# Optimization experiments

Hardware: AMD Instinct MI355X
Metric: run time of the kernel (lower is better)

Reference implementation:

```python
import jax, jax.numpy as jnp
import numpy as np

B, S, H, E, TOP_K = 4, 4096, 4096, 64, 2

def setup_inputs() -> dict:
    key = jax.random.key(0)
    k1, k2 = jax.random.split(key)
    hidden_states = jax.random.normal(k1, (B, S, H), dtype=jnp.float32)
    gate_weight = jax.random.normal(k2, (E, H), dtype=jnp.float32) * (H ** -0.5)
    return {"hidden_states": hidden_states, "gate_weight": gate_weight}

def reference(hidden_states, gate_weight):
    # gate: logits[b,s,e] = hidden[b,s,h] @ W[e,h]^T (nn.Linear, no bias)
    router_logits = jnp.einsum('bsh,eh->bse', hidden_states, gate_weight)
    router_probs = jax.nn.softmax(router_logits, axis=-1)
    # top-k over experts, then renormalize the selected weights
    expert_weights, expert_indices = jax.lax.top_k(router_probs, TOP_K)
    expert_weights = expert_weights / jnp.sum(expert_weights, axis=-1, keepdims=True)
    return (router_probs, expert_indices, expert_weights)
```

## Files before the change

kernel.cpp:

```cpp
#include <hip/hip_runtime.h>
#include <math.h>

#define TOKENS 16384
#define HDIM 4096
#define NE 64

#define BM 64
#define BK 32
#define KSPLIT 8
#define KSLICE (HDIM / KSPLIT)
#define LDSP 68

__global__ __launch_bounds__(256, 4) void router_gemm(const float* __restrict__ A,
                                                      const float* __restrict__ W,
                                                      float* __restrict__ P) {
  __shared__ float As[BK * LDSP];
  __shared__ float Ws[BK * LDSP];

  const int tid = threadIdx.x;
  const int bt = blockIdx.x;
  const int ks = blockIdx.y;

  const int sr = tid >> 2;
  const int sc = (tid & 3) * 4;

  const float* Ab = A + (size_t)(bt * BM + sr) * HDIM + (size_t)ks * KSLICE + sc;
  const float* Wb = W + (size_t)sr * HDIM + (size_t)ks * KSLICE + sc;

  const int tx = tid & 15;
  const int ty = tid >> 4;

  float acc[4][4];
#pragma unroll
  for (int i = 0; i < 4; ++i)
#pragma unroll
    for (int j = 0; j < 4; ++j) acc[i][j] = 0.f;

  float4 a0 = *(const float4*)(Ab);
  float4 a1 = *(const float4*)(Ab + 16);
  float4 w0 = *(const float4*)(Wb);
  float4 w1 = *(const float4*)(Wb + 16);

  for (int kc = 0; kc < KSLICE; kc += BK) {
    As[(sc + 0) * LDSP + sr] = a0.x;
    As[(sc + 1) * LDSP + sr] = a0.y;
    As[(sc + 2) * LDSP + sr] = a0.z;
    As[(sc + 3) * LDSP + sr] = a0.w;
    As[(sc + 16) * LDSP + sr] = a1.x;
    As[(sc + 17) * LDSP + sr] = a1.y;
    As[(sc + 18) * LDSP + sr] = a1.z;
    As[(sc + 19) * LDSP + sr] = a1.w;
    Ws[(sc + 0) * LDSP + sr] = w0.x;
    Ws[(sc + 1) * LDSP + sr] = w0.y;
    Ws[(sc + 2) * LDSP + sr] = w0.z;
    Ws[(sc + 3) * LDSP + sr] = w0.w;
    Ws[(sc + 16) * LDSP + sr] = w1.x;
    Ws[(sc + 17) * LDSP + sr] = w1.y;
    Ws[(sc + 18) * LDSP + sr] = w1.z;
    Ws[(sc + 19) * LDSP + sr] = w1.w;
    __syncthreads();

    if (kc + BK < KSLICE) {
      a0 = *(const float4*)(Ab + kc + BK);
      a1 = *(const float4*)(Ab + kc + BK + 16);
      w0 = *(const float4*)(Wb + kc + BK);
      w1 = *(const float4*)(Wb + kc + BK + 16);
    }

#pragma unroll
    for (int k = 0; k < BK; ++k) {
      float4 av = *(const float4*)&As[k * LDSP + ty * 4];
      float4 wv = *(const float4*)&Ws[k * LDSP + tx * 4];
      const float a[4] = {av.x, av.y, av.z, av.w};
      const float w[4] = {wv.x, wv.y, wv.z, wv.w};
#pragma unroll
      for (int i = 0; i < 4; ++i)
#pragma unroll
        for (int j = 0; j < 4; ++j) acc[i][j] = fmaf(a[i], w[j], acc[i][j]);
    }
    __syncthreads();
  }

  float* Pb = P + ((size_t)ks * TOKENS + (size_t)bt * BM + ty * 4) * NE + tx * 4;
#pragma unroll
  for (int i = 0; i < 4; ++i)
    *(float4*)(Pb + (size_t)i * NE) =
        make_float4(acc[i][0], acc[i][1], acc[i][2], acc[i][3]);
}

__global__ __launch_bounds__(256) void router_finalize(const float* __restrict__ P,
                                                       float* __restrict__ out) {
  const int lane = threadIdx.x & 63;
  const int wave = threadIdx.x >> 6;
  const int tok = blockIdx.x * 4 + wave;

  float l = 0.f;
#pragma unroll
  for (int s = 0; s < KSPLIT; ++s)
    l += P[((size_t)s * TOKENS + tok) * NE + lane];

  float m = l;
#pragma unroll
  for (int off = 32; off >= 1; off >>= 1) m = fmaxf(m, __shfl_xor(m, off, 64));

  const float e = expf(l - m);
  float sum = e;
#pragma unroll
  for (int off = 32; off >= 1; off >>= 1) sum += __shfl_xor(sum, off, 64);

  const float p = e / sum;
  out[(size_t)tok * NE + lane] = p;

  float m0 = p;
#pragma unroll
  for (int off = 32; off >= 1; off >>= 1) m0 = fmaxf(m0, __shfl_xor(m0, off, 64));
  const unsigned long long b0 = __ballot(p == m0);
  const int i0 = __ffsll(b0) - 1;

  const float pm = (lane == i0) ? -1.f : p;
  float m1 = pm;
#pragma unroll
  for (int off = 32; off >= 1; off >>= 1) m1 = fmaxf(m1, __shfl_xor(m1, off, 64));
  const unsigned long long b1 = __ballot(pm == m1);
  const int i1 = __ffsll(b1) - 1;

  if (lane == 0) {
    float* idxo = out + (size_t)TOKENS * NE + (size_t)tok * 2;
    idxo[0] = (float)i0;
    idxo[1] = (float)i1;
    float* wo = out + (size_t)TOKENS * NE + (size_t)TOKENS * 2 + (size_t)tok * 2;
    const float d = m0 + m1;
    wo[0] = m0 / d;
    wo[1] = m1 / d;
  }
}

extern "C" void kernel_launch(void* const* d_in, const int* in_sizes, int n_in,
                              void* d_out, int out_size, void* d_ws, size_t ws_size,
                              hipStream_t stream) {
  const float* A = (const float*)d_in[0];
  const float* W = (const float*)d_in[1];
  float* out = (float*)d_out;
  float* P = (float*)d_ws;

  dim3 gridA(TOKENS / BM, KSPLIT);
  router_gemm<<<gridA, 256, 0, stream>>>(A, W, P);
  router_finalize<<<TOKENS / 4, 256, 0, stream>>>(P, out);
}
```

Measured before the change: 397.4 us.

## Fuse router GEMM and softmax/top-k into one kernel with in-block K split

Replaces the 8-way split-K GEMM plus separate finalize kernel with a single kernel. Each 512-thread block covers 64 tokens and splits K across two 256-thread halves, then reduces the two partial sums in shared memory. Softmax and top-2 selection run in the same block straight from LDS. This removes the workspace round trip and the second launch. In exchange the grid shrinks to 256 blocks with a longer serial K loop, which lowers parallelism and latency hiding.

```diff
diff --git a/kernel.cpp b/kernel.cpp
--- a/kernel.cpp
+++ b/kernel.cpp
@@ -7,28 +7,32 @@
 
 #define BM 64
 #define BK 32
-#define KSPLIT 8
-#define KSLICE (HDIM / KSPLIT)
+#define NKG 2
+#define KSLICE (HDIM / NKG)
 #define LDSP 68
+#define TILE (BK * LDSP)
 
-__global__ __launch_bounds__(256, 4) void router_gemm(const float* __restrict__ A,
-                                                      const float* __restrict__ W,
-                                                      float* __restrict__ P) {
-  __shared__ float As[BK * LDSP];
-  __shared__ float Ws[BK * LDSP];
+__global__ __launch_bounds__(512, 2) void router_fused(const float* __restrict__ A,
+                                                       const float* __restrict__ W,
+                                                       float* __restrict__ out) {
+  __shared__ float smem[NKG * 2 * TILE];
 
   const int tid = threadIdx.x;
+  const int kg = tid >> 8;
+  const int t = tid & 255;
   const int bt = blockIdx.x;
-  const int ks = blockIdx.y;
 
-  const int sr = tid >> 2;
-  const int sc = (tid & 3) * 4;
+  const int sr = t >> 2;
+  const int sc = (t & 3) * 4;
 
-  const float* Ab = A + (size_t)(bt * BM + sr) * HDIM + (size_t)ks * KSLICE + sc;
-  const float* Wb = W + (size_t)sr * HDIM + (size_t)ks * KSLICE + sc;
+  const float* Ab = A + (size_t)(bt * BM + sr) * HDIM + (size_t)kg * KSLICE + sc;
+  const float* Wb = W + (size_t)sr * HDIM + (size_t)kg * KSLICE + sc;
 
-  const int tx = tid & 15;
-  const int ty = tid >> 4;
+  float* As = smem + kg * (2 * TILE);
+  float* Ws = As + TILE;
+
+  const int tx = t & 15;
+  const int ty = t >> 4;
 
   float acc[4][4];
 #pragma unroll
@@ -81,57 +85,67 @@
     __syncthreads();
   }
 
-  float* Pb = P + ((size_t)ks * TOKENS + (size_t)bt * BM + ty * 4) * NE + tx * 4;
+  float* L = smem;
+  if (kg == 0) {
 #pragma unroll
-  for (int i = 0; i < 4; ++i)
-    *(float4*)(Pb + (size_t)i * NE) =
-        make_float4(acc[i][0], acc[i][1], acc[i][2], acc[i][3]);
-}
+    for (int i = 0; i < 4; ++i)
+      *(float4*)&L[(ty * 4 + i) * LDSP + tx * 4] =
+          make_float4(acc[i][0], acc[i][1], acc[i][2], acc[i][3]);
+  }
+  __syncthreads();
+  if (kg == 1) {
+#pragma unroll
+    for (int i = 0; i < 4; ++i) {
+      float4* p = (float4*)&L[(ty * 4 + i) * LDSP + tx * 4];
+      float4 v = *p;
+      *p = make_float4(v.x + acc[i][0], v.y + acc[i][1], v.z + acc[i][2],
+                       v.w + acc[i][3]);
+    }
+  }
+  __syncthreads();
 
-__global__ __launch_bounds__(256) void router_finalize(const float* __restrict__ P,
-                                                       float* __restrict__ out) {
-  const int lane = threadIdx.x & 63;
-  const int wave = threadIdx.x >> 6;
-  const int tok = blockIdx.x * 4 + wave;
+  const int lane = tid & 63;
+  const int wv8 = tid >> 6;
+#pragma unroll
+  for (int r = 0; r < 8; ++r) {
+    const int lt = wv8 * 8 + r;
+    const int tok = bt * BM + lt;
+    const float l = L[lt * LDSP + lane];
 
-  float l = 0.f;
+    float m = l;
 #pragma unroll
-  for (int s = 0; s < KSPLIT; ++s)
-    l += P[((size_t)s * TOKENS + tok) * NE + lane];
+    for (int off = 32; off >= 1; off >>= 1) m = fmaxf(m, __shfl_xor(m, off, 64));
 
-  float m = l;
+    const float e = expf(l - m);
+    float sum = e;
 #pragma unroll
-  for (int off = 32; off >= 1; off >>= 1) m = fmaxf(m, __shfl_xor(m, off, 64));
+    for (int off = 32; off >= 1; off >>= 1) sum += __shfl_xor(sum, off, 64);
 
-  const float e = expf(l - m);
-  float sum = e;
+    const float p = e / sum;
+    out[(size_t)tok * NE + lane] = p;
+
+    float m0 = p;
 #pragma unroll
-  for (int off = 32; off >= 1; off >>= 1) sum += __shfl_xor(sum, off, 64);
+    for (int off = 32; off >= 1; off >>= 1) m0 = fmaxf(m0, __shfl_xor(m0, off, 64));
+    const unsigned long long b0 = __ballot(p == m0);
+    const int i0 = __ffsll(b0) - 1;
 
-  const float p = e / sum;
-  out[(size_t)tok * NE + lane] = p;
+    const float pm = (lane == i0) ? -1.f : p;
+    float m1 = pm;
+#pragma unroll
+    for (int off = 32; off >= 1; off >>= 1) m1 = fmaxf(m1, __shfl_xor(m1, off, 64));
+    const unsigned long long b1 = __ballot(pm == m1);
+    const int i1 = __ffsll(b1) - 1;
 
-  float m0 = p;
-#pragma unroll
-  for (int off = 32; off >= 1; off >>= 1) m0 = fmaxf(m0, __shfl_xor(m0, off, 64));
-  const unsigned long long b0 = __ballot(p == m0);
-  const int i0 = __ffsll(b0) - 1;
-
-  const float pm = (lane == i0) ? -1.f : p;
-  float m1 = pm;
-#pragma unroll
-  for (int off = 32; off >= 1; off >>= 1) m1 = fmaxf(m1, __shfl_xor(m1, off, 64));
-  const unsigned long long b1 = __ballot(pm == m1);
-  const int i1 = __ffsll(b1) - 1;
-
-  if (lane == 0) {
-    float* idxo = out + (size_t)TOKENS * NE + (size_t)tok * 2;
-    idxo[0] = (float)i0;
-    idxo[1] = (float)i1;
-    float* wo = out + (size_t)TOKENS * NE + (size_t)TOKENS * 2 + (size_t)tok * 2;
-    const float d = m0 + m1;
-    wo[0] = m0 / d;
-    wo[1] = m1 / d;
+    if (lane == 0) {
+      float* idxo = out + (size_t)TOKENS * NE + (size_t)tok * 2;
+      idxo[0] = (float)i0;
+      idxo[1] = (float)i1;
+      float* wo = out + (size_t)TOKENS * NE + (size_t)TOKENS * 2 + (size_t)tok * 2;
+      const float d = m0 + m1;
+      wo[0] = m0 / d;
+      wo[1] = m1 / d;
+    }
   }
 }
 
@@ -141,9 +155,7 @@
   const float* A = (const float*)d_in[0];
   const float* W = (const float*)d_in[1];
   float* out = (float*)d_out;
-  float* P = (float*)d_ws;
+  (void)d_ws;
 
-  dim3 gridA(TOKENS / BM, KSPLIT);
-  router_gemm<<<gridA, 256, 0, stream>>>(A, W, P);
-  router_finalize<<<TOKENS / 4, 256, 0, stream>>>(P, out);
+  router_fused<<<dim3(TOKENS / BM), 512, 0, stream>>>(A, W, out);
 }
```

New measurement: 395.5 us. Within noise of the previous version (-0.5%).
